# Performance work log

Hardware: AMD Instinct MI355X
Metric: run time of the kernel (lower is better)

Reference implementation:

```python
import jax, jax.numpy as jnp
import numpy as np

B, K, T, H, D = 16, 49, 256, 512, 512


def setup_inputs() -> dict:
    key = jax.random.key(0)
    ks = jax.random.split(key, 8)
    s = 1.0 / np.sqrt(H)
    return {
        "V": jax.random.normal(ks[0], (B, K, H), jnp.float32),
        "h_t": jax.random.normal(ks[1], (B, T, H), jnp.float32),
        "s_t": jax.random.normal(ks[2], (B, T, H), jnp.float32),
        "Wv": jax.random.normal(ks[3], (H, D), jnp.float32) * s,
        "bv": jnp.zeros((D,), jnp.float32),
        "Wg": jax.random.normal(ks[4], (H, D), jnp.float32) * s,
        "bg": jnp.zeros((D,), jnp.float32),
        "Ws": jax.random.normal(ks[5], (H, D), jnp.float32) * s,
        "bs": jnp.zeros((D,), jnp.float32),
        "Wh": jax.random.normal(ks[6], (D, 1), jnp.float32) * (1.0 / np.sqrt(D)),
        "bh": jnp.zeros((1,), jnp.float32),
    }


def reference(V, h_t, s_t, Wv, bv, Wg, bg, Ws, bs, Wh, bh):
    # projections (dropout is identity in eval)
    cv = V @ Wv + bv                        # [B, K, D]
    cg = h_t @ Wg + bg                      # [B, T, D]
    # content_v: [B, T, K, D] via broadcast add
    content_v = cv[:, None, :, :] + cg[:, :, None, :]
    z_t = (jnp.tanh(content_v) @ Wh + bh)[..., 0]   # [B, T, K]
    alpha_t = jax.nn.softmax(z_t, axis=-1)          # [B, T, K]
    c_t = jnp.einsum('btk,bkh->bth', alpha_t, V)    # [B, T, H]
    # sentinel branch
    content_s = (s_t @ Ws + bs) + cg                # [B, T, D]
    z_ext = jnp.tanh(content_s) @ Wh + bh           # [B, T, 1]
    extended = jnp.concatenate([z_t, z_ext], axis=-1)  # [B, T, K+1]
    alpha_hat = jax.nn.softmax(extended, axis=-1)
    beta_t = alpha_hat[:, :, -1:]                   # [B, T, 1]
    c_hat_t = beta_t * s_t + (1.0 - beta_t) * c_t   # [B, T, H]
    return (c_hat_t, alpha_t, beta_t)
```

## Files before the change

### kernel.cpp

```cpp
#include <hip/hip_runtime.h>
#include <hip/hip_fp16.h>
#include <cstdint>
#include <cstddef>

#define B_ 16
#define K_ 49
#define T_ 256
#define H_ 512
#define D_ 512

#define TANH_SCALE 2.8853900817779268f
#define LOG2E 1.4426950408889634f

typedef _Float16 half8 __attribute__((ext_vector_type(8)));
typedef float floatx4 __attribute__((ext_vector_type(4)));

#define ROWS_A 9088
#define OFF_V 0
#define OFF_H 896
#define OFF_S 4992

__device__ __forceinline__ void async16(const _Float16* g, const _Float16* l) {
    __builtin_amdgcn_global_load_lds(
        (const __attribute__((address_space(1))) unsigned int*)g,
        (__attribute__((address_space(3))) unsigned int*)l, 16, 0, 0);
}

__global__ __launch_bounds__(256) void conv_all(const float* __restrict__ V,
                                                const float* __restrict__ h_t,
                                                const float* __restrict__ s_t,
                                                const float* __restrict__ Wv,
                                                const float* __restrict__ Wg,
                                                const float* __restrict__ Ws,
                                                _Float16* __restrict__ Af16,
                                                _Float16* __restrict__ Wt) {
    __shared__ float tile[32][33];
    int tid = threadIdx.x;
    if (blockIdx.x < 2272) {
        int idx = (blockIdx.x * 256 + tid) * 8;
        int row = idx >> 9;
        int col = idx & 511;
        const float* src;
        if (row < 784)        src = V   + (size_t)row * 512 + col;
        else if (row < 896)   src = nullptr;
        else if (row < 4992)  src = h_t + (size_t)(row - 896) * 512 + col;
        else                  src = s_t + (size_t)(row - 4992) * 512 + col;
        half8 h;
        if (src) {
            float4 f0 = *(const float4*)(src);
            float4 f1 = *(const float4*)(src + 4);
            h[0] = (_Float16)f0.x; h[1] = (_Float16)f0.y;
            h[2] = (_Float16)f0.z; h[3] = (_Float16)f0.w;
            h[4] = (_Float16)f1.x; h[5] = (_Float16)f1.y;
            h[6] = (_Float16)f1.z; h[7] = (_Float16)f1.w;
        } else {
            h = (half8)((_Float16)0.0f);
        }
        *(half8*)(Af16 + idx) = h;
    } else {
        int bid = blockIdx.x - 2272;
        int p = bid >> 8;
        int rem = bid & 255;
        int bx = rem & 15, by = rem >> 4;
        const float* W = (p == 0) ? Wv : (p == 1) ? Wg : Ws;
        _Float16* outp = Wt + (size_t)p * 512 * 512;
        int tx = tid & 31, ty = tid >> 5;
        int c = bx * 32 + tx;
        int rbase = by * 32;
#pragma unroll
        for (int i = 0; i < 4; i++)
            tile[ty + i * 8][tx] = W[(size_t)(rbase + ty + i * 8) * 512 + c];
        __syncthreads();
        int k = rbase + tx;
#pragma unroll
        for (int i = 0; i < 4; i++) {
            int n = bx * 32 + ty + i * 8;
            outp[(size_t)n * 512 + k] = (_Float16)(tile[tx][ty + i * 8] * TANH_SCALE);
        }
    }
}

__global__ __launch_bounds__(256) void gemm_f16(
    const _Float16* __restrict__ Af16, const _Float16* __restrict__ Wt,
    const float* __restrict__ bv, const float* __restrict__ bg2,
    const float* __restrict__ bs, float* __restrict__ cv,
    float* __restrict__ cg, float* __restrict__ cs) {
    __shared__ __align__(16) _Float16 As[64 * 64];
    __shared__ __align__(16) _Float16 Bs[64 * 64];

    int id = blockIdx.x;
    int rowbase; const _Float16* Bt; const float* bias; float* C;
    if (id < 112)       { rowbase = OFF_V;            Bt = Wt;          bias = bv;  C = cv; }
    else if (id < 624)  { id -= 112; rowbase = OFF_H; Bt = Wt + 262144; bias = bg2; C = cg; }
    else                { id -= 624; rowbase = OFF_S; Bt = Wt + 524288; bias = bs;  C = cs; }
    int tm = id >> 3, tn = id & 7;

    int tid = threadIdx.x;
    int wave = tid >> 6, lane = tid & 63;

    const _Float16* gA[2]; int ldsA[2];
    const _Float16* gB[2]; int ldsB[2];
#pragma unroll
    for (int i = 0; i < 2; i++) {
        int p = i * 256 + tid;
        int ks = p >> 8, x = (p >> 6) & 3, q = (p >> 4) & 3, f = p & 15;
        gA[i] = Af16 + (size_t)(rowbase + tm * 64 + x * 16 + f) * 512 + ks * 32 + q * 8;
        gB[i] = Bt   + (size_t)(tn * 64 + x * 16 + f) * 512 + ks * 32 + q * 8;
        ldsA[i] = p * 8;
        ldsB[i] = p * 8;
    }

    floatx4 acc[4];
#pragma unroll
    for (int x = 0; x < 4; x++) acc[x] = (floatx4)0.0f;

    for (int kk = 0; kk < 8; kk++) {
        if (kk) __syncthreads();
#pragma unroll
        for (int i = 0; i < 2; i++) async16(gA[i] + kk * 64, &As[ldsA[i]]);
#pragma unroll
        for (int i = 0; i < 2; i++) async16(gB[i] + kk * 64, &Bs[ldsB[i]]);
        __syncthreads();

#pragma unroll
        for (int ks = 0; ks < 2; ks++) {
            half8 a[4];
#pragma unroll
            for (int x = 0; x < 4; x++)
                a[x] = *(const half8*)&As[(ks * 256 + x * 64 + lane) * 8];
            half8 b = *(const half8*)&Bs[(ks * 256 + wave * 64 + lane) * 8];
#pragma unroll
            for (int x = 0; x < 4; x++)
                acc[x] = __builtin_amdgcn_mfma_f32_16x16x32_f16(a[x], b, acc[x], 0, 0, 0);
        }
    }

    int dn = lane & 15, dq = lane >> 4;
    int colg = tn * 64 + wave * 16 + dn;
    float bc = bias[colg] * TANH_SCALE;
#pragma unroll
    for (int x = 0; x < 4; x++) {
        int rowg = tm * 64 + x * 16 + dq * 4;
#pragma unroll
        for (int r = 0; r < 4; r++)
            C[(size_t)(rowg + r) * 512 + colg] = __builtin_amdgcn_exp2f(acc[x][r] + bc);
    }
}

__device__ __forceinline__ float wave_sum(float v) {
#pragma unroll
    for (int o = 32; o > 0; o >>= 1) v += __shfl_xor(v, o);
    return v;
}
__device__ __forceinline__ float wave_max(float v) {
#pragma unroll
    for (int o = 32; o > 0; o >>= 1) v = fmaxf(v, __shfl_xor(v, o));
    return v;
}

__device__ __forceinline__ float xsum4(float a0, float a1, float a2, float a3, int lane) {
    bool hi = (lane & 32) != 0;
    float t0 = hi ? a0 : a2;
    float t1 = hi ? a1 : a3;
    t0 = __shfl_xor(t0, 32);
    t1 = __shfl_xor(t1, 32);
    if (hi) { a0 = t0; a1 = t1; } else { a2 = t0; a3 = t1; }
    bool h2 = (lane & 16) != 0;
    float u0 = h2 ? a0 : a1;
    float u1 = h2 ? a2 : a3;
    u0 = __shfl_xor(u0, 16);
    u1 = __shfl_xor(u1, 16);
    if (h2) { a0 = u0; a2 = u1; } else { a1 = u0; a3 = u1; }
    float s = (a0 + a1) + (a2 + a3);
#pragma unroll
    for (int o = 8; o > 0; o >>= 1) s += __shfl_xor(s, o);
    return s;
}

#define TB 4
__global__ __launch_bounds__(256) void z_kernel(
    const float* __restrict__ ecv, const float* __restrict__ ecg,
    const float* __restrict__ ecs, const float* __restrict__ V,
    const float* __restrict__ s_t, const float* __restrict__ Wh,
    const float* __restrict__ bh, float* __restrict__ out) {
    int bx = blockIdx.x;
    int b  = bx >> 6;
    int t0 = (bx & 63) << 2;
    int bt0 = b * 256 + t0;
    int tid = threadIdx.x;
    int wave = tid >> 6, lane = tid & 63;

    __shared__ float zl[TB][64];
    __shared__ float4 al4[52];
    __shared__ float bl[TB];

    float whv[8], egv[TB][8];
#pragma unroll
    for (int j = 0; j < 8; j++) whv[j] = Wh[j * 64 + lane];
#pragma unroll
    for (int tt = 0; tt < TB; tt++) {
        const float* cgp = ecg + (size_t)(bt0 + tt) * 512;
#pragma unroll
        for (int j = 0; j < 8; j++) egv[tt][j] = cgp[j * 64 + lane];
    }
    float s8 = 0.0f;
#pragma unroll
    for (int j = 0; j < 8; j++) s8 += whv[j];
    float zbase = wave_sum(s8) + bh[0];

    float rv[8], rn[8];
    {
        const float* rp = ecv + (size_t)(b * 49 + wave) * 512;
#pragma unroll
        for (int j = 0; j < 8; j++) rv[j] = rp[j * 64 + lane];
    }
    for (int task = wave; task < 49; task += 4) {
        int nt = task + 4;
        if (nt < 49) {
            const float* rp = ecv + (size_t)(b * 49 + nt) * 512;
#pragma unroll
            for (int j = 0; j < 8; j++) rn[j] = rp[j * 64 + lane];
        }
        float acc[TB] = {0.0f, 0.0f, 0.0f, 0.0f};
#pragma unroll
        for (int tt = 0; tt < TB; tt++) {
#pragma unroll
            for (int j = 0; j < 8; j++) {
                float t = fmaf(rv[j], egv[tt][j], 1.0f);
                float r = __builtin_amdgcn_rcpf(t);
                acc[tt] = fmaf(whv[j], r, acc[tt]);
            }
        }
        float z = xsum4(acc[0], acc[1], acc[2], acc[3], lane);
        if ((lane & 15) == 0) zl[lane >> 4][task] = zbase - 2.0f * z;
#pragma unroll
        for (int j = 0; j < 8; j++) rv[j] = rn[j];
    }
#pragma unroll
    for (int tt = 0; tt < TB; tt++) {
        if (wave == tt) {
            const float* rp = ecs + (size_t)(bt0 + tt) * 512;
            float acc = 0.0f;
#pragma unroll
            for (int j = 0; j < 8; j++) {
                float t = fmaf(rp[j * 64 + lane], egv[tt][j], 1.0f);
                float r = __builtin_amdgcn_rcpf(t);
                acc = fmaf(whv[j], r, acc);
            }
            float s = wave_sum(acc);
            if (lane == 0) zl[tt][49] = zbase - 2.0f * s;
        }
    }
    __syncthreads();

    {
        int w = wave;
        float z = (lane < 49) ? zl[w][lane] : -3.0e38f;
        float m = wave_max(z);
        float e = (lane < 49) ? __builtin_amdgcn_exp2f((z - m) * LOG2E) : 0.0f;
        float s = wave_sum(e);
        float zext = zl[w][49];
        float m2 = fmaxf(m, zext);
        float sc   = __builtin_amdgcn_exp2f((m - m2) * LOG2E);
        float eext = __builtin_amdgcn_exp2f((zext - m2) * LOG2E);
        float s2 = s * sc + eext;
        float beta = eext / s2;
        if (lane < 49) {
            float a = e / s;
            ((float*)&al4[lane])[w] = a;
            out[(size_t)B_ * T_ * H_ + (size_t)(bt0 + w) * 49 + lane] = a;
        }
        if (lane == 0) {
            bl[w] = beta;
            out[(size_t)B_ * T_ * H_ + (size_t)B_ * T_ * K_ + (bt0 + w)] = beta;
        }
    }
    __syncthreads();

    const float* Vb = V + (size_t)b * 49 * 512;
    float2 accA[TB];
#pragma unroll
    for (int tt = 0; tt < TB; tt++) accA[tt] = make_float2(0.0f, 0.0f);
#pragma unroll 7
    for (int k = 0; k < 49; k++) {
        float4 a4 = al4[k];
        float2 v = *(const float2*)(Vb + (size_t)k * 512 + tid * 2);
        accA[0].x = fmaf(a4.x, v.x, accA[0].x);  accA[0].y = fmaf(a4.x, v.y, accA[0].y);
        accA[1].x = fmaf(a4.y, v.x, accA[1].x);  accA[1].y = fmaf(a4.y, v.y, accA[1].y);
        accA[2].x = fmaf(a4.z, v.x, accA[2].x);  accA[2].y = fmaf(a4.z, v.y, accA[2].y);
        accA[3].x = fmaf(a4.w, v.x, accA[3].x);  accA[3].y = fmaf(a4.w, v.y, accA[3].y);
    }
#pragma unroll
    for (int tt = 0; tt < TB; tt++) {
        float beta = bl[tt];
        float2 sp = *(const float2*)(s_t + (size_t)(bt0 + tt) * 512 + tid * 2);
        float2 o;
        o.x = beta * sp.x + (1.0f - beta) * accA[tt].x;
        o.y = beta * sp.y + (1.0f - beta) * accA[tt].y;
        *(float2*)(out + (size_t)(bt0 + tt) * 512 + tid * 2) = o;
    }
}

extern "C" void kernel_launch(void* const* d_in, const int* in_sizes, int n_in,
                              void* d_out, int out_size, void* d_ws, size_t ws_size,
                              hipStream_t stream) {
    const float* V   = (const float*)d_in[0];
    const float* h_t = (const float*)d_in[1];
    const float* s_t = (const float*)d_in[2];
    const float* Wv  = (const float*)d_in[3];
    const float* bv  = (const float*)d_in[4];
    const float* Wg  = (const float*)d_in[5];
    const float* bg  = (const float*)d_in[6];
    const float* Ws  = (const float*)d_in[7];
    const float* bs  = (const float*)d_in[8];
    const float* Wh  = (const float*)d_in[9];
    const float* bh  = (const float*)d_in[10];
    float* out = (float*)d_out;

    char* ws = (char*)d_ws;
    _Float16* Af16 = (_Float16*)(ws);
    _Float16* Wt   = (_Float16*)(ws + 9306112);
    float* ecv = (float*)(ws + 10878976);
    float* ecg = (float*)(ws + 12713984);
    float* ecs = (float*)(ws + 21102592);

    conv_all<<<3040, 256, 0, stream>>>(V, h_t, s_t, Wv, Wg, Ws, Af16, Wt);
    gemm_f16<<<1136, 256, 0, stream>>>(Af16, Wt, bv, bg, bs, ecv, ecg, ecs);
    z_kernel<<<1024, 256, 0, stream>>>(ecv, ecg, ecs, V, s_t, Wh, bh, out);
}
```

Before: 135.1 us.

## Fuse conversion, GEMM and attention stages into one cooperative persistent kernel

Replaces the three separate launches (fp16 conversion/weight transpose, MFMA projection GEMM, attention/softmax kernel) with a single cooperative kernel of 512 persistent blocks. The blocks loop over each stage's work items and separate the stages with grid-wide syncs. This is meant to remove per-launch overhead and the tail gaps between kernels. In exchange it adds two grid barriers and pays with reduced parallelism per stage: 512 blocks loop over 1136 GEMM tiles and 1024 attention tasks, which may cause load imbalance. If the cooperative launch fails it falls back to the old three-kernel path.

```diff
diff --git a/kernel.cpp b/kernel.cpp
--- a/kernel.cpp
+++ b/kernel.cpp
@@ -1,7 +1,10 @@
 #include <hip/hip_runtime.h>
+#include <hip/hip_cooperative_groups.h>
 #include <hip/hip_fp16.h>
 #include <cstdint>
 #include <cstddef>
+
+namespace cg = cooperative_groups;
 
 #define B_ 16
 #define K_ 49
@@ -15,7 +18,6 @@
 typedef _Float16 half8 __attribute__((ext_vector_type(8)));
 typedef float floatx4 __attribute__((ext_vector_type(4)));
 
-#define ROWS_A 9088
 #define OFF_V 0
 #define OFF_H 896
 #define OFF_S 4992
@@ -24,6 +26,281 @@
     __builtin_amdgcn_global_load_lds(
         (const __attribute__((address_space(1))) unsigned int*)g,
         (__attribute__((address_space(3))) unsigned int*)l, 16, 0, 0);
+}
+
+__device__ __forceinline__ float wave_sum(float v) {
+#pragma unroll
+    for (int o = 32; o > 0; o >>= 1) v += __shfl_xor(v, o);
+    return v;
+}
+__device__ __forceinline__ float wave_max(float v) {
+#pragma unroll
+    for (int o = 32; o > 0; o >>= 1) v = fmaxf(v, __shfl_xor(v, o));
+    return v;
+}
+__device__ __forceinline__ float xsum4(float a0, float a1, float a2, float a3, int lane) {
+    bool hi = (lane & 32) != 0;
+    float t0 = hi ? a0 : a2;
+    float t1 = hi ? a1 : a3;
+    t0 = __shfl_xor(t0, 32);
+    t1 = __shfl_xor(t1, 32);
+    if (hi) { a0 = t0; a1 = t1; } else { a2 = t0; a3 = t1; }
+    bool h2 = (lane & 16) != 0;
+    float u0 = h2 ? a0 : a1;
+    float u1 = h2 ? a2 : a3;
+    u0 = __shfl_xor(u0, 16);
+    u1 = __shfl_xor(u1, 16);
+    if (h2) { a0 = u0; a2 = u1; } else { a1 = u0; a3 = u1; }
+    float s = (a0 + a1) + (a2 + a3);
+#pragma unroll
+    for (int o = 8; o > 0; o >>= 1) s += __shfl_xor(s, o);
+    return s;
+}
+
+#define TB 4
+
+__global__ __launch_bounds__(256, 4) void fused_all(
+    const float* __restrict__ V, const float* __restrict__ h_t,
+    const float* __restrict__ s_t, const float* __restrict__ Wv,
+    const float* __restrict__ Wg, const float* __restrict__ Ws,
+    const float* __restrict__ bv, const float* __restrict__ bg2,
+    const float* __restrict__ bs, const float* __restrict__ Wh,
+    const float* __restrict__ bh, _Float16* __restrict__ Af16,
+    _Float16* __restrict__ Wt, float* __restrict__ ecv,
+    float* __restrict__ ecg, float* __restrict__ ecs,
+    float* __restrict__ out)
+{
+    extern __shared__ __align__(16) char smem[];
+    cg::grid_group grid = cg::this_grid();
+    int blk = blockIdx.x;
+    int nblk = gridDim.x;
+    int tid = threadIdx.x;
+    int wave = tid >> 6, lane = tid & 63;
+
+    for (int c = blk * 256 + tid; c < 581632; c += nblk * 256) {
+        int idx = c * 8;
+        int row = idx >> 9;
+        int col = idx & 511;
+        const float* src;
+        if (row < 784)        src = V   + (size_t)row * 512 + col;
+        else if (row < 896)   src = nullptr;
+        else if (row < 4992)  src = h_t + (size_t)(row - 896) * 512 + col;
+        else                  src = s_t + (size_t)(row - 4992) * 512 + col;
+        half8 h;
+        if (src) {
+            float4 f0 = *(const float4*)(src);
+            float4 f1 = *(const float4*)(src + 4);
+            h[0] = (_Float16)f0.x; h[1] = (_Float16)f0.y;
+            h[2] = (_Float16)f0.z; h[3] = (_Float16)f0.w;
+            h[4] = (_Float16)f1.x; h[5] = (_Float16)f1.y;
+            h[6] = (_Float16)f1.z; h[7] = (_Float16)f1.w;
+        } else {
+            h = (half8)((_Float16)0.0f);
+        }
+        *(half8*)(Af16 + idx) = h;
+    }
+    for (int wt = blk; wt < 768; wt += nblk) {
+        __syncthreads();
+        float* tile = (float*)smem;
+        int p = wt >> 8;
+        int rem = wt & 255;
+        int bx = rem & 15, by = rem >> 4;
+        const float* W = (p == 0) ? Wv : (p == 1) ? Wg : Ws;
+        _Float16* outp = Wt + (size_t)p * 512 * 512;
+        int tx = tid & 31, ty = tid >> 5;
+        int c = bx * 32 + tx;
+        int rbase = by * 32;
+#pragma unroll
+        for (int i = 0; i < 4; i++)
+            tile[(ty + i * 8) * 33 + tx] = W[(size_t)(rbase + ty + i * 8) * 512 + c];
+        __syncthreads();
+        int k = rbase + tx;
+#pragma unroll
+        for (int i = 0; i < 4; i++) {
+            int n = bx * 32 + ty + i * 8;
+            outp[(size_t)n * 512 + k] = (_Float16)(tile[tx * 33 + ty + i * 8] * TANH_SCALE);
+        }
+    }
+    grid.sync();
+
+    {
+        _Float16* As = (_Float16*)smem;
+        _Float16* Bs = As + 4096;
+        for (int tile_id = blk; tile_id < 1136; tile_id += nblk) {
+            __syncthreads();
+
+            int id = tile_id;
+            int rowbase; const _Float16* Bt; const float* bias; float* C;
+            if (id < 112)       { rowbase = OFF_V;            Bt = Wt;          bias = bv;  C = ecv; }
+            else if (id < 624)  { id -= 112; rowbase = OFF_H; Bt = Wt + 262144; bias = bg2; C = ecg; }
+            else                { id -= 624; rowbase = OFF_S; Bt = Wt + 524288; bias = bs;  C = ecs; }
+            int tm = id >> 3, tn = id & 7;
+
+            const _Float16* gA[2]; const _Float16* gB[2]; int ldsA[2];
+#pragma unroll
+            for (int i = 0; i < 2; i++) {
+                int p = i * 256 + tid;
+                int ks = p >> 8, x = (p >> 6) & 3, q = (p >> 4) & 3, f = p & 15;
+                gA[i] = Af16 + (size_t)(rowbase + tm * 64 + x * 16 + f) * 512 + ks * 32 + q * 8;
+                gB[i] = Bt   + (size_t)(tn * 64 + x * 16 + f) * 512 + ks * 32 + q * 8;
+                ldsA[i] = p * 8;
+            }
+
+            floatx4 acc[4];
+#pragma unroll
+            for (int x = 0; x < 4; x++) acc[x] = (floatx4)0.0f;
+
+            for (int kk = 0; kk < 8; kk++) {
+                if (kk) __syncthreads();
+#pragma unroll
+                for (int i = 0; i < 2; i++) async16(gA[i] + kk * 64, As + ldsA[i]);
+#pragma unroll
+                for (int i = 0; i < 2; i++) async16(gB[i] + kk * 64, Bs + ldsA[i]);
+                __syncthreads();
+
+#pragma unroll
+                for (int ks = 0; ks < 2; ks++) {
+                    half8 a[4];
+#pragma unroll
+                    for (int x = 0; x < 4; x++)
+                        a[x] = *(const half8*)&As[(ks * 256 + x * 64 + lane) * 8];
+                    half8 b = *(const half8*)&Bs[(ks * 256 + wave * 64 + lane) * 8];
+#pragma unroll
+                    for (int x = 0; x < 4; x++)
+                        acc[x] = __builtin_amdgcn_mfma_f32_16x16x32_f16(a[x], b, acc[x], 0, 0, 0);
+                }
+            }
+
+            int dn = lane & 15, dq = lane >> 4;
+            int colg = tn * 64 + wave * 16 + dn;
+            float bc = bias[colg] * TANH_SCALE;
+#pragma unroll
+            for (int x = 0; x < 4; x++) {
+                int rowg = tm * 64 + x * 16 + dq * 4;
+#pragma unroll
+                for (int r = 0; r < 4; r++)
+                    C[(size_t)(rowg + r) * 512 + colg] = __builtin_amdgcn_exp2f(acc[x][r] + bc);
+            }
+        }
+    }
+    grid.sync();
+
+    for (int task = blk; task < 1024; task += nblk) {
+        __syncthreads();
+        float*  zl  = (float*)smem;
+        float4* al4 = (float4*)(smem + 1024);
+        float*  bl  = (float*)(smem + 1856);
+
+        int b  = task >> 6;
+        int t0 = (task & 63) << 2;
+        int bt0 = b * 256 + t0;
+
+        float whv[8], egv[TB][8];
+#pragma unroll
+        for (int j = 0; j < 8; j++) whv[j] = Wh[j * 64 + lane];
+#pragma unroll
+        for (int tt = 0; tt < TB; tt++) {
+            const float* cgp = ecg + (size_t)(bt0 + tt) * 512;
+#pragma unroll
+            for (int j = 0; j < 8; j++) egv[tt][j] = cgp[j * 64 + lane];
+        }
+        float s8 = 0.0f;
+#pragma unroll
+        for (int j = 0; j < 8; j++) s8 += whv[j];
+        float zbase = wave_sum(s8) + bh[0];
+
+        float rv[8], rn[8];
+        {
+            const float* rp = ecv + (size_t)(b * 49 + wave) * 512;
+#pragma unroll
+            for (int j = 0; j < 8; j++) rv[j] = rp[j * 64 + lane];
+        }
+        for (int tk = wave; tk < 49; tk += 4) {
+            int nt = tk + 4;
+            if (nt < 49) {
+                const float* rp = ecv + (size_t)(b * 49 + nt) * 512;
+#pragma unroll
+                for (int j = 0; j < 8; j++) rn[j] = rp[j * 64 + lane];
+            }
+            float acc[TB] = {0.0f, 0.0f, 0.0f, 0.0f};
+#pragma unroll
+            for (int tt = 0; tt < TB; tt++) {
+#pragma unroll
+                for (int j = 0; j < 8; j++) {
+                    float t = fmaf(rv[j], egv[tt][j], 1.0f);
+                    float r = __builtin_amdgcn_rcpf(t);
+                    acc[tt] = fmaf(whv[j], r, acc[tt]);
+                }
+            }
+            float z = xsum4(acc[0], acc[1], acc[2], acc[3], lane);
+            if ((lane & 15) == 0) zl[(lane >> 4) * 64 + tk] = zbase - 2.0f * z;
+#pragma unroll
+            for (int j = 0; j < 8; j++) rv[j] = rn[j];
+        }
+#pragma unroll
+        for (int tt = 0; tt < TB; tt++) {
+            if (wave == tt) {
+                const float* rp = ecs + (size_t)(bt0 + tt) * 512;
+                float acc = 0.0f;
+#pragma unroll
+                for (int j = 0; j < 8; j++) {
+                    float t = fmaf(rp[j * 64 + lane], egv[tt][j], 1.0f);
+                    float r = __builtin_amdgcn_rcpf(t);
+                    acc = fmaf(whv[j], r, acc);
+                }
+                float s = wave_sum(acc);
+                if (lane == 0) zl[tt * 64 + 49] = zbase - 2.0f * s;
+            }
+        }
+        __syncthreads();
+
+        {
+            int w = wave;
+            float z = (lane < 49) ? zl[w * 64 + lane] : -3.0e38f;
+            float m = wave_max(z);
+            float e = (lane < 49) ? __builtin_amdgcn_exp2f((z - m) * LOG2E) : 0.0f;
+            float s = wave_sum(e);
+            float zext = zl[w * 64 + 49];
+            float m2 = fmaxf(m, zext);
+            float sc   = __builtin_amdgcn_exp2f((m - m2) * LOG2E);
+            float eext = __builtin_amdgcn_exp2f((zext - m2) * LOG2E);
+            float s2 = s * sc + eext;
+            float beta = eext / s2;
+            if (lane < 49) {
+                float a = e / s;
+                ((float*)(al4 + lane))[w] = a;
+                out[(size_t)B_ * T_ * H_ + (size_t)(bt0 + w) * 49 + lane] = a;
+            }
+            if (lane == 0) {
+                bl[w] = beta;
+                out[(size_t)B_ * T_ * H_ + (size_t)B_ * T_ * K_ + (bt0 + w)] = beta;
+            }
+        }
+        __syncthreads();
+
+        const float* Vb = V + (size_t)b * 49 * 512;
+        float2 accA[TB];
+#pragma unroll
+        for (int tt = 0; tt < TB; tt++) accA[tt] = make_float2(0.0f, 0.0f);
+#pragma unroll 7
+        for (int k = 0; k < 49; k++) {
+            float4 a4 = al4[k];
+            float2 v = *(const float2*)(Vb + (size_t)k * 512 + tid * 2);
+            accA[0].x = fmaf(a4.x, v.x, accA[0].x);  accA[0].y = fmaf(a4.x, v.y, accA[0].y);
+            accA[1].x = fmaf(a4.y, v.x, accA[1].x);  accA[1].y = fmaf(a4.y, v.y, accA[1].y);
+            accA[2].x = fmaf(a4.z, v.x, accA[2].x);  accA[2].y = fmaf(a4.z, v.y, accA[2].y);
+            accA[3].x = fmaf(a4.w, v.x, accA[3].x);  accA[3].y = fmaf(a4.w, v.y, accA[3].y);
+        }
+#pragma unroll
+        for (int tt = 0; tt < TB; tt++) {
+            float beta = bl[tt];
+            float2 sp = *(const float2*)(s_t + (size_t)(bt0 + tt) * 512 + tid * 2);
+            float2 o;
+            o.x = beta * sp.x + (1.0f - beta) * accA[tt].x;
+            o.y = beta * sp.y + (1.0f - beta) * accA[tt].y;
+            *(float2*)(out + (size_t)(bt0 + tt) * 512 + tid * 2) = o;
+        }
+    }
 }
 
 __global__ __launch_bounds__(256) void conv_all(const float* __restrict__ V,
@@ -84,22 +361,21 @@
     const _Float16* __restrict__ Af16, const _Float16* __restrict__ Wt,
     const float* __restrict__ bv, const float* __restrict__ bg2,
     const float* __restrict__ bs, float* __restrict__ cv,
-    float* __restrict__ cg, float* __restrict__ cs) {
+    float* __restrict__ cg2, float* __restrict__ cs) {
     __shared__ __align__(16) _Float16 As[64 * 64];
     __shared__ __align__(16) _Float16 Bs[64 * 64];
 
     int id = blockIdx.x;
     int rowbase; const _Float16* Bt; const float* bias; float* C;
     if (id < 112)       { rowbase = OFF_V;            Bt = Wt;          bias = bv;  C = cv; }
-    else if (id < 624)  { id -= 112; rowbase = OFF_H; Bt = Wt + 262144; bias = bg2; C = cg; }
+    else if (id < 624)  { id -= 112; rowbase = OFF_H; Bt = Wt + 262144; bias = bg2; C = cg2; }
     else                { id -= 624; rowbase = OFF_S; Bt = Wt + 524288; bias = bs;  C = cs; }
     int tm = id >> 3, tn = id & 7;
 
     int tid = threadIdx.x;
     int wave = tid >> 6, lane = tid & 63;
 
-    const _Float16* gA[2]; int ldsA[2];
-    const _Float16* gB[2]; int ldsB[2];
+    const _Float16* gA[2]; const _Float16* gB[2]; int ldsA[2];
 #pragma unroll
     for (int i = 0; i < 2; i++) {
         int p = i * 256 + tid;
@@ -107,7 +383,6 @@
         gA[i] = Af16 + (size_t)(rowbase + tm * 64 + x * 16 + f) * 512 + ks * 32 + q * 8;
         gB[i] = Bt   + (size_t)(tn * 64 + x * 16 + f) * 512 + ks * 32 + q * 8;
         ldsA[i] = p * 8;
-        ldsB[i] = p * 8;
     }
 
     floatx4 acc[4];
@@ -117,9 +392,9 @@
     for (int kk = 0; kk < 8; kk++) {
         if (kk) __syncthreads();
 #pragma unroll
-        for (int i = 0; i < 2; i++) async16(gA[i] + kk * 64, &As[ldsA[i]]);
-#pragma unroll
-        for (int i = 0; i < 2; i++) async16(gB[i] + kk * 64, &Bs[ldsB[i]]);
+        for (int i = 0; i < 2; i++) async16(gA[i] + kk * 64, As + ldsA[i]);
+#pragma unroll
+        for (int i = 0; i < 2; i++) async16(gB[i] + kk * 64, Bs + ldsA[i]);
         __syncthreads();
 
 #pragma unroll
@@ -147,37 +422,6 @@
     }
 }
 
-__device__ __forceinline__ float wave_sum(float v) {
-#pragma unroll
-    for (int o = 32; o > 0; o >>= 1) v += __shfl_xor(v, o);
-    return v;
-}
-__device__ __forceinline__ float wave_max(float v) {
-#pragma unroll
-    for (int o = 32; o > 0; o >>= 1) v = fmaxf(v, __shfl_xor(v, o));
-    return v;
-}
-
-__device__ __forceinline__ float xsum4(float a0, float a1, float a2, float a3, int lane) {
-    bool hi = (lane & 32) != 0;
-    float t0 = hi ? a0 : a2;
-    float t1 = hi ? a1 : a3;
-    t0 = __shfl_xor(t0, 32);
-    t1 = __shfl_xor(t1, 32);
-    if (hi) { a0 = t0; a1 = t1; } else { a2 = t0; a3 = t1; }
-    bool h2 = (lane & 16) != 0;
-    float u0 = h2 ? a0 : a1;
-    float u1 = h2 ? a2 : a3;
-    u0 = __shfl_xor(u0, 16);
-    u1 = __shfl_xor(u1, 16);
-    if (h2) { a0 = u0; a2 = u1; } else { a1 = u0; a3 = u1; }
-    float s = (a0 + a1) + (a2 + a3);
-#pragma unroll
-    for (int o = 8; o > 0; o >>= 1) s += __shfl_xor(s, o);
-    return s;
-}
-
-#define TB 4
 __global__ __launch_bounds__(256) void z_kernel(
     const float* __restrict__ ecv, const float* __restrict__ ecg,
     const float* __restrict__ ecs, const float* __restrict__ V,
@@ -324,7 +568,15 @@
     float* ecg = (float*)(ws + 12713984);
     float* ecs = (float*)(ws + 21102592);
 
-    conv_all<<<3040, 256, 0, stream>>>(V, h_t, s_t, Wv, Wg, Ws, Af16, Wt);
-    gemm_f16<<<1136, 256, 0, stream>>>(Af16, Wt, bv, bg, bs, ecv, ecg, ecs);
-    z_kernel<<<1024, 256, 0, stream>>>(ecv, ecg, ecs, V, s_t, Wh, bh, out);
-}
+    void* args[] = {(void*)&V, (void*)&h_t, (void*)&s_t, (void*)&Wv, (void*)&Wg,
+                    (void*)&Ws, (void*)&bv, (void*)&bg, (void*)&bs, (void*)&Wh,
+                    (void*)&bh, (void*)&Af16, (void*)&Wt, (void*)&ecv, (void*)&ecg,
+                    (void*)&ecs, (void*)&out};
+    hipError_t err = hipLaunchCooperativeKernel((void*)fused_all, dim3(512), dim3(256),
+                                                args, 16384, stream);
+    if (err != hipSuccess) {
+        conv_all<<<3040, 256, 0, stream>>>(V, h_t, s_t, Wv, Wg, Ws, Af16, Wt);
+        gemm_f16<<<1136, 256, 0, stream>>>(Af16, Wt, bv, bg, bs, ecv, ecg, ecs);
+        z_kernel<<<1024, 256, 0, stream>>>(ecv, ecg, ecs, V, s_t, Wh, bh, out);
+    }
+}
```

Result: slower. 284.8 us (+110.9%).
